# Performance work log

Measured on AMD Instinct MI355X. Metric: run time of the kernel, lower is better.

The kernel has to match this reference:

```python
import jax, jax.numpy as jnp
import numpy as np

N_NODES = 50000
N_EDGES = 800000
IN_DIM, HID_DIM, OUT_DIM, N_CLASSES = 128, 256, 64, 40


def _xavier(key, shape):
    fan_in, fan_out = shape[0], shape[1]
    std = float(np.sqrt(2.0 / (fan_in + fan_out)))
    return jax.random.normal(key, shape, dtype=jnp.float32) * std


def gcn_conv(x, W, b, src, dst, n_nodes):
    """PyG GCNConv: add self-loops, symmetric D^-1/2 (A+I) D^-1/2 X W + b."""
    h = x @ W  # [N, out]
    loop = jnp.arange(n_nodes, dtype=src.dtype)
    s = jnp.concatenate([src, loop])  # sources (messages flow src -> dst)
    d = jnp.concatenate([dst, loop])
    ones = jnp.ones(s.shape[0], dtype=h.dtype)
    deg = jax.ops.segment_sum(ones, d, num_segments=n_nodes)  # in-degree incl. self-loop
    dinv = jnp.where(deg > 0, jax.lax.rsqrt(deg), 0.0)
    norm = dinv[s] * dinv[d]  # [E+N]
    msg = h[s] * norm[:, None]
    out = jax.ops.segment_sum(msg, d, num_segments=n_nodes)
    return out + b


def setup_inputs() -> dict:
    key = jax.random.key(0)
    ks = jax.random.split(key, 9)
    x = jax.random.normal(ks[0], (N_NODES, IN_DIM), dtype=jnp.float32)
    edge_index = jax.random.randint(ks[1], (2, N_EDGES), 0, N_NODES, dtype=jnp.int64)
    return {
        "x": x,
        "edge_index": edge_index,
        "W1": _xavier(ks[2], (IN_DIM, HID_DIM)),
        "b1": jnp.zeros((HID_DIM,), jnp.float32),
        "W2": _xavier(ks[3], (HID_DIM, OUT_DIM)),
        "b2": jnp.zeros((OUT_DIM,), jnp.float32),
        "Wp1": _xavier(ks[4], (2 * OUT_DIM, 4 * OUT_DIM)),
        "bp1": jnp.zeros((4 * OUT_DIM,), jnp.float32),
        "Wp2": _xavier(ks[5], (4 * OUT_DIM, OUT_DIM)),
        "bp2": jnp.zeros((OUT_DIM,), jnp.float32),
        "Wc": _xavier(ks[6], (OUT_DIM, N_CLASSES)),
        "bc": jnp.zeros((N_CLASSES,), jnp.float32),
    }


def reference(x, edge_index, W1, b1, W2, b2, Wp1, bp1, Wp2, bp2, Wc, bc):
    src, dst = edge_index[0], edge_index[1]
    n = x.shape[0]
    h = jax.nn.relu(gcn_conv(x, W1, b1, src, dst, n))  # [N, HID]
    f = gcn_conv(h, W2, b2, src, dst, n)  # [N, OUT]
    # edge MLP on gathered endpoint features
    ef = jnp.concatenate([f[src], f[dst]], axis=-1)  # [E, 2*OUT]
    ef = jax.nn.relu(ef @ Wp1 + bp1)  # [E, 4*OUT]
    edge_feats = ef @ Wp2 + bp2  # [E, OUT]
    logits = f @ Wc + bc  # [N, C]
    return f, edge_feats, logits, edge_index
```

## Files before the change

kernel.cpp:

```cpp
#include <hip/hip_runtime.h>

#define N_NODES   50000
#define N_EDGES   800000
#define IN_DIM    128
#define HID_DIM   256
#define OUT_DIM   64
#define N_CLASSES 40

typedef __attribute__((ext_vector_type(8))) short short8;
typedef __attribute__((ext_vector_type(8))) unsigned short ushort8;
typedef __attribute__((ext_vector_type(4))) float f32x4;

__device__ inline short f2bf(float x) {
    unsigned u = __builtin_bit_cast(unsigned, x);
    unsigned r = (u + 0x7FFFu + ((u >> 16) & 1u)) >> 16;
    return (short)r;
}
__device__ inline float bf2f(unsigned short u) {
    unsigned v = ((unsigned)u) << 16;
    return __builtin_bit_cast(float, v);
}
__device__ inline unsigned cvtpk(float lo, float hi) {
    unsigned r;
    asm("v_cvt_pk_bf16_f32 %0, %1, %2" : "=v"(r) : "v"(lo), "v"(hi));
    return r;
}
__device__ __host__ inline int swap23(int p) {
    return (p & 0xC3) | ((p >> 2) & 0x0C) | ((p << 2) & 0x30);
}


__global__ void k_prep(const float* __restrict__ x, const int* __restrict__ ei,
                       const float* __restrict__ W1, const float* __restrict__ W2,
                       const float* __restrict__ Wp1, const float* __restrict__ Wp2,
                       unsigned short* __restrict__ xb,
                       short* __restrict__ W1t, short* __restrict__ W2t,
                       short* __restrict__ Wp1t, short* __restrict__ Wp2t,
                       int* __restrict__ degi, int* __restrict__ cursor,
                       float* __restrict__ ei_out) {
    int i = blockIdx.x * 256 + threadIdx.x;
    if (i < N_NODES) { degi[i] = 0; cursor[i] = 0; }
    if (i < 128 * 256) {
        int k = i >> 8, n = i & 255;
        W1t[n * 128 + k]  = f2bf(W1[i]);
        Wp1t[n * 128 + k] = f2bf(Wp1[i]);
    }
    if (i < 256 * 64) {
        int p = i >> 6, o = i & 63;
        int h = swap23(p);
        W2t[o * 256 + p]  = f2bf(W2[h * 64 + o]);
        Wp2t[o * 256 + p] = f2bf(Wp2[h * 64 + o]);
    }
    if (i < N_NODES * IN_DIM / 4) {
        float4 v = ((const float4*)x)[i];
        uint2 u;
        u.x = cvtpk(v.x, v.y);
        u.y = cvtpk(v.z, v.w);
        *(uint2*)((unsigned short*)xb + (size_t)i * 4) = u;
    }
    if (i < (2 * N_EDGES) / 4) {
        int4 v = ((const int4*)ei)[i];
        float4 o = {(float)v.x, (float)v.y, (float)v.z, (float)v.w};
        ((float4*)ei_out)[i] = o;
    }
}


__global__ void k_deg_count(const int* __restrict__ dst, int* __restrict__ degi) {
    int e = blockIdx.x * 256 + threadIdx.x;
    if (e < N_EDGES) atomicAdd(&degi[dst[e]], 1);
}

__global__ void k_scan_bsum(const int* __restrict__ vals, int n, int* __restrict__ bsum,
                            float* __restrict__ dinv) {
    __shared__ int sm[256];
    int t = threadIdx.x, i = blockIdx.x * 256 + t;
    int d = (i < n) ? vals[i] : 0;
    if (i < n) dinv[i] = rsqrtf((float)(d + 1));
    sm[t] = d;
    __syncthreads();
    for (int s = 128; s > 0; s >>= 1) {
        if (t < s) sm[t] += sm[t + s];
        __syncthreads();
    }
    if (t == 0) bsum[blockIdx.x] = sm[0];
}

__global__ void k_scan_bscan(int* __restrict__ bsum, int nb) {
    __shared__ int sm[256];
    int t = threadIdx.x;
    int orig = (t < nb) ? bsum[t] : 0;
    sm[t] = orig;
    __syncthreads();
    for (int off = 1; off < 256; off <<= 1) {
        int v = (t >= off) ? sm[t - off] : 0;
        __syncthreads();
        sm[t] += v;
        __syncthreads();
    }
    if (t < nb) bsum[t] = sm[t] - orig;
}

__global__ void k_scan_final(const int* __restrict__ vals, int n,
                             const int* __restrict__ bscan, int* __restrict__ out) {
    __shared__ int sm[256];
    int t = threadIdx.x, i = blockIdx.x * 256 + t;
    int orig = (i < n) ? vals[i] : 0;
    sm[t] = orig;
    __syncthreads();
    for (int off = 1; off < 256; off <<= 1) {
        int v = (t >= off) ? sm[t - off] : 0;
        __syncthreads();
        sm[t] += v;
        __syncthreads();
    }
    int excl = sm[t] - orig + bscan[blockIdx.x];
    if (i < n) out[i] = excl;
    if (i == n - 1) out[n] = excl + orig;
}

__global__ void k_csr_fill(const int* __restrict__ src, const int* __restrict__ dst,
                           const int* __restrict__ csr_off, int* __restrict__ cursor,
                           int* __restrict__ csr_src) {
    int e = blockIdx.x * 256 + threadIdx.x;
    if (e < N_EDGES) {
        int d = dst[e];
        int pos = csr_off[d] + atomicAdd(&cursor[d], 1);
        csr_src[pos] = src[e];
    }
}


__global__ __launch_bounds__(256) void k_agg0(const unsigned short* __restrict__ xb,
                                              const float* __restrict__ dinv,
                                              const int* __restrict__ csr_off,
                                              const int* __restrict__ csr_src,
                                              unsigned short* __restrict__ xa) {
    const int v = blockIdx.x * 4 + (threadIdx.x >> 6);
    const int lane = threadIdx.x & 63;
    float dv = dinv[v];
    unsigned c = *(const unsigned*)(xb + (size_t)v * 128 + lane * 2);
    float a0 = bf2f((unsigned short)(c & 0xFFFF)) * dv;
    float a1 = bf2f((unsigned short)(c >> 16)) * dv;
    int beg = csr_off[v], end = csr_off[v + 1];
    for (int base = beg; base < end; base += 64) {
        int idx = base + lane;
        int sj = (idx < end) ? csr_src[idx] : 0;
        float dj = (idx < end) ? dinv[sj] : 0.f;
        int m = min(64, end - base);
        int j = 0;
        for (; j + 4 <= m; j += 4) {
            int s0 = __shfl(sj, j), s1 = __shfl(sj, j + 1);
            int s2 = __shfl(sj, j + 2), s3 = __shfl(sj, j + 3);
            float d0 = __shfl(dj, j), d1 = __shfl(dj, j + 1);
            float d2 = __shfl(dj, j + 2), d3 = __shfl(dj, j + 3);
            unsigned h0 = *(const unsigned*)(xb + (size_t)s0 * 128 + lane * 2);
            unsigned h1 = *(const unsigned*)(xb + (size_t)s1 * 128 + lane * 2);
            unsigned h2 = *(const unsigned*)(xb + (size_t)s2 * 128 + lane * 2);
            unsigned h3 = *(const unsigned*)(xb + (size_t)s3 * 128 + lane * 2);
            a0 += bf2f((unsigned short)(h0 & 0xFFFF)) * d0 + bf2f((unsigned short)(h1 & 0xFFFF)) * d1
                + bf2f((unsigned short)(h2 & 0xFFFF)) * d2 + bf2f((unsigned short)(h3 & 0xFFFF)) * d3;
            a1 += bf2f((unsigned short)(h0 >> 16)) * d0 + bf2f((unsigned short)(h1 >> 16)) * d1
                + bf2f((unsigned short)(h2 >> 16)) * d2 + bf2f((unsigned short)(h3 >> 16)) * d3;
        }
        for (; j < m; j++) {
            int s = __shfl(sj, j);
            float ds = __shfl(dj, j);
            unsigned hv = *(const unsigned*)(xb + (size_t)s * 128 + lane * 2);
            a0 += bf2f((unsigned short)(hv & 0xFFFF)) * ds;
            a1 += bf2f((unsigned short)(hv >> 16)) * ds;
        }
    }
    *(unsigned*)(xa + (size_t)v * 128 + lane * 2) = cvtpk(a0 * dv, a1 * dv);
}


__global__ __launch_bounds__(256) void k_agg2(const unsigned short* __restrict__ h2b,
                                              const float* __restrict__ dinv,
                                              const int* __restrict__ csr_off,
                                              const int* __restrict__ csr_src,
                                              const float* __restrict__ b2,
                                              const float* __restrict__ Wc,
                                              const float* __restrict__ bc,
                                              float* __restrict__ f_out,
                                              unsigned short* __restrict__ fb,
                                              float* __restrict__ lg_out) {
    const int v = blockIdx.x * 4 + (threadIdx.x >> 6);
    const int lane = threadIdx.x & 63;
    float dv = dinv[v];
    float acc = bf2f(h2b[(size_t)v * 64 + lane]) * dv;
    int beg = csr_off[v], end = csr_off[v + 1];
    for (int base = beg; base < end; base += 64) {
        int idx = base + lane;
        int sj = (idx < end) ? csr_src[idx] : 0;
        float dj = (idx < end) ? dinv[sj] : 0.f;
        int m = min(64, end - base);
        int j = 0;
        for (; j + 4 <= m; j += 4) {
            int s0 = __shfl(sj, j), s1 = __shfl(sj, j + 1);
            int s2 = __shfl(sj, j + 2), s3 = __shfl(sj, j + 3);
            float d0 = __shfl(dj, j), d1 = __shfl(dj, j + 1);
            float d2 = __shfl(dj, j + 2), d3 = __shfl(dj, j + 3);
            float h0 = bf2f(h2b[(size_t)s0 * 64 + lane]);
            float h1 = bf2f(h2b[(size_t)s1 * 64 + lane]);
            float h2 = bf2f(h2b[(size_t)s2 * 64 + lane]);
            float h3 = bf2f(h2b[(size_t)s3 * 64 + lane]);
            acc += h0 * d0 + h1 * d1 + h2 * d2 + h3 * d3;
        }
        for (; j < m; j++) {
            int s = __shfl(sj, j);
            float ds = __shfl(dj, j);
            acc += bf2f(h2b[(size_t)s * 64 + lane]) * ds;
        }
    }
    float r = acc * dv + b2[lane];
    f_out[(size_t)v * 64 + lane] = r;
    fb[(size_t)v * 64 + lane] = (unsigned short)f2bf(r);
    bool act = lane < N_CLASSES;
    float lacc = act ? bc[lane] : 0.f;
    #pragma unroll
    for (int i2 = 0; i2 < 64; i2++) {
        float fi = __shfl(r, i2);
        if (act) lacc += fi * Wc[i2 * N_CLASSES + lane];
    }
    if (act) lg_out[(size_t)v * N_CLASSES + lane] = lacc;
}


__global__ __launch_bounds__(256) void k_gemm12(const unsigned short* __restrict__ xa,
                                                const short* __restrict__ W1t,
                                                const float* __restrict__ b1,
                                                const short* __restrict__ W2t,
                                                unsigned short* __restrict__ h2b) {
    __shared__ unsigned short xs[64 * 128];
    __shared__ unsigned short hs[64 * 256];
    const int t = threadIdx.x;
    const int lane = t & 63, wv = t >> 6, lr = lane & 15, lg = lane >> 4;
    const int nb = blockIdx.x * 64;

    #pragma unroll
    for (int i = 0; i < 4; i++) {
        int q = t + i * 256, row = q >> 4, seg = q & 15;
        int node = nb + row;
        ushort8 v = {0, 0, 0, 0, 0, 0, 0, 0};
        if (node < N_NODES) v = *(const ushort8*)(xa + (size_t)node * 128 + seg * 8);
        *(ushort8*)((char*)xs + ((row * 256 + seg * 16) ^ ((row & 7) << 4))) = v;
    }

    short8 A1[4][4];
    #pragma unroll
    for (int mi = 0; mi < 4; mi++)
        #pragma unroll
        for (int kt = 0; kt < 4; kt++)
            A1[mi][kt] = *(const short8*)(W1t + (size_t)(wv * 64 + mi * 16 + lr) * 128 + kt * 32 + lg * 8);
    float4 bb1[4];
    #pragma unroll
    for (int mi = 0; mi < 4; mi++)
        bb1[mi] = *(const float4*)(b1 + wv * 64 + mi * 16 + lg * 4);
    __syncthreads();

    #pragma unroll
    for (int nj = 0; nj < 4; nj++) {
        short8 Bf[4];
        int nr = nj * 16 + lr;
        #pragma unroll
        for (int kt = 0; kt < 4; kt++)
            Bf[kt] = *(const short8*)((const char*)xs + ((nr * 256 + kt * 64 + lg * 16) ^ ((nr & 7) << 4)));
        #pragma unroll
        for (int mh = 0; mh < 2; mh++) {
            f32x4 a0 = {0.f, 0.f, 0.f, 0.f}, a1 = {0.f, 0.f, 0.f, 0.f};
            #pragma unroll
            for (int kt = 0; kt < 4; kt++) {
                a0 = __builtin_amdgcn_mfma_f32_16x16x32_bf16(A1[mh * 2 + 0][kt], Bf[kt], a0, 0, 0, 0);
                a1 = __builtin_amdgcn_mfma_f32_16x16x32_bf16(A1[mh * 2 + 1][kt], Bf[kt], a1, 0, 0, 0);
            }
            float4 b0 = bb1[mh * 2 + 0], b1v = bb1[mh * 2 + 1];
            uint4 pkv;
            pkv.x = cvtpk(fmaxf(a0[0] + b0.x, 0.f),  fmaxf(a0[1] + b0.y, 0.f));
            pkv.y = cvtpk(fmaxf(a0[2] + b0.z, 0.f),  fmaxf(a0[3] + b0.w, 0.f));
            pkv.z = cvtpk(fmaxf(a1[0] + b1v.x, 0.f), fmaxf(a1[1] + b1v.y, 0.f));
            pkv.w = cvtpk(fmaxf(a1[2] + b1v.z, 0.f), fmaxf(a1[3] + b1v.w, 0.f));
            *(uint4*)((char*)hs + ((nr * 512 + wv * 128 + lg * 32 + mh * 16) ^ ((nr & 7) << 4))) = pkv;
        }
    }

    short8 A2[8];
    #pragma unroll
    for (int kt = 0; kt < 8; kt++)
        A2[kt] = *(const short8*)(W2t + (size_t)(wv * 16 + lr) * 256 + kt * 32 + lg * 8);
    asm volatile("s_waitcnt lgkmcnt(0)" ::: "memory");
    __builtin_amdgcn_s_barrier();

    #pragma unroll
    for (int nj = 0; nj < 4; nj++) {
        short8 Bh[8];
        int nr = nj * 16 + lr;
        #pragma unroll
        for (int kt = 0; kt < 8; kt++)
            Bh[kt] = *(const short8*)((const char*)hs + ((nr * 512 + kt * 64 + lg * 16) ^ ((nr & 7) << 4)));
        int node = nb + nr;
        f32x4 acc = {0.f, 0.f, 0.f, 0.f};
        #pragma unroll
        for (int kt = 0; kt < 8; kt++)
            acc = __builtin_amdgcn_mfma_f32_16x16x32_bf16(A2[kt], Bh[kt], acc, 0, 0, 0);
        if (node < N_NODES) {
            uint2 u;
            u.x = cvtpk(acc[0], acc[1]);
            u.y = cvtpk(acc[2], acc[3]);
            *(uint2*)(h2b + (size_t)node * 64 + wv * 16 + lg * 4) = u;
        }
    }
}


__global__ __launch_bounds__(256) void k_edge_mlpC(
        const unsigned short* __restrict__ fb,
        const int* __restrict__ src, const int* __restrict__ dst,
        const short* __restrict__ Wp1t, const float* __restrict__ bp1,
        const short* __restrict__ Wp2t, const float* __restrict__ bp2,
        float* __restrict__ out, int n_tiles) {
    __shared__ unsigned short hid_s[2][32 * 256];

    const int t = threadIdx.x;
    const int lane = t & 63, wv = t >> 6, lr = lane & 15, lg = lane >> 4;

    short8 A1[4][4];
    #pragma unroll
    for (int mi = 0; mi < 4; mi++)
        #pragma unroll
        for (int kt = 0; kt < 4; kt++)
            A1[mi][kt] = *(const short8*)(Wp1t + (size_t)(wv * 64 + mi * 16 + lr) * 128 + kt * 32 + lg * 8);
    short8 A2[8];
    #pragma unroll
    for (int kt = 0; kt < 8; kt++)
        A2[kt] = *(const short8*)(Wp2t + (size_t)(wv * 16 + lr) * 256 + kt * 32 + lg * 8);
    float4 bb1[4];
    #pragma unroll
    for (int mi = 0; mi < 4; mi++)
        bb1[mi] = *(const float4*)(bp1 + wv * 64 + mi * 16 + lg * 4);
    const float4 bv2 = *(const float4*)(bp2 + wv * 16 + lg * 4);

    int tile = blockIdx.x;
    if (tile >= n_tiles) return;
    const int g = gridDim.x;

    short8 Bf[2][4];
    {
        int sC[2], dC[2];
        #pragma unroll
        for (int nj = 0; nj < 2; nj++) {
            int e = tile * 32 + nj * 16 + lr;
            sC[nj] = src[e];
            dC[nj] = dst[e];
        }
        #pragma unroll
        for (int nj = 0; nj < 2; nj++) {
            const unsigned short* srow = fb + (size_t)sC[nj] * 64;
            const unsigned short* drow = fb + (size_t)dC[nj] * 64;
            Bf[nj][0] = *(const short8*)(srow + lg * 8);
            Bf[nj][1] = *(const short8*)(srow + 32 + lg * 8);
            Bf[nj][2] = *(const short8*)(drow + lg * 8);
            Bf[nj][3] = *(const short8*)(drow + 32 + lg * 8);
        }
    }
    int sA[2], dA[2];
    {
        int tn = tile + g;
        if (tn < n_tiles) {
            #pragma unroll
            for (int nj = 0; nj < 2; nj++) {
                int e = tn * 32 + nj * 16 + lr;
                sA[nj] = src[e];
                dA[nj] = dst[e];
            }
        }
    }

    int cur = 0;
    for (; tile < n_tiles; tile += g) {
        #pragma unroll
        for (int nj = 0; nj < 2; nj++) {
            int er = nj * 16 + lr;
            #pragma unroll
            for (int mh = 0; mh < 2; mh++) {
                f32x4 a0 = {0.f, 0.f, 0.f, 0.f}, a1 = {0.f, 0.f, 0.f, 0.f};
                #pragma unroll
                for (int kt = 0; kt < 4; kt++) {
                    a0 = __builtin_amdgcn_mfma_f32_16x16x32_bf16(A1[mh * 2 + 0][kt], Bf[nj][kt], a0, 0, 0, 0);
                    a1 = __builtin_amdgcn_mfma_f32_16x16x32_bf16(A1[mh * 2 + 1][kt], Bf[nj][kt], a1, 0, 0, 0);
                }
                float4 b0 = bb1[mh * 2 + 0], b1v = bb1[mh * 2 + 1];
                uint4 pkv;
                pkv.x = cvtpk(fmaxf(a0[0] + b0.x, 0.f),  fmaxf(a0[1] + b0.y, 0.f));
                pkv.y = cvtpk(fmaxf(a0[2] + b0.z, 0.f),  fmaxf(a0[3] + b0.w, 0.f));
                pkv.z = cvtpk(fmaxf(a1[0] + b1v.x, 0.f), fmaxf(a1[1] + b1v.y, 0.f));
                pkv.w = cvtpk(fmaxf(a1[2] + b1v.z, 0.f), fmaxf(a1[3] + b1v.w, 0.f));
                *(uint4*)((char*)hid_s[cur] +
                    ((er * 512 + wv * 128 + lg * 32 + mh * 16) ^ ((er & 7) << 4))) = pkv;
            }
        }

        int tn = tile + g;
        if (tn < n_tiles) {
            #pragma unroll
            for (int nj = 0; nj < 2; nj++) {
                const unsigned short* srow = fb + (size_t)sA[nj] * 64;
                const unsigned short* drow = fb + (size_t)dA[nj] * 64;
                Bf[nj][0] = *(const short8*)(srow + lg * 8);
                Bf[nj][1] = *(const short8*)(srow + 32 + lg * 8);
                Bf[nj][2] = *(const short8*)(drow + lg * 8);
                Bf[nj][3] = *(const short8*)(drow + 32 + lg * 8);
            }
        }
        int tnn = tile + 2 * g;
        if (tnn < n_tiles) {
            #pragma unroll
            for (int nj = 0; nj < 2; nj++) {
                int e = tnn * 32 + nj * 16 + lr;
                sA[nj] = src[e];
                dA[nj] = dst[e];
            }
        }

        asm volatile("s_waitcnt lgkmcnt(0)" ::: "memory");
        __builtin_amdgcn_s_barrier();

        #pragma unroll
        for (int nj = 0; nj < 2; nj++) {
            short8 Bh[8];
            int er = nj * 16 + lr;
            #pragma unroll
            for (int kt = 0; kt < 8; kt++)
                Bh[kt] = *(const short8*)((const char*)hid_s[cur] +
                             ((er * 512 + kt * 64 + lg * 16) ^ ((er & 7) << 4)));
            f32x4 acc = {0.f, 0.f, 0.f, 0.f};
            #pragma unroll
            for (int kt = 0; kt < 8; kt++)
                acc = __builtin_amdgcn_mfma_f32_16x16x32_bf16(A2[kt], Bh[kt], acc, 0, 0, 0);
            float4 o = {acc[0] + bv2.x, acc[1] + bv2.y, acc[2] + bv2.z, acc[3] + bv2.w};
            *(float4*)(out + (size_t)(tile * 32 + er) * 64 + wv * 16 + lg * 4) = o;
        }
        cur ^= 1;
    }
}


extern "C" void kernel_launch(void* const* d_in, const int* in_sizes, int n_in,
                              void* d_out, int out_size, void* d_ws, size_t ws_size,
                              hipStream_t stream) {
    const float* x   = (const float*)d_in[0];
    const int*   ei  = (const int*)d_in[1];
    const float* W1  = (const float*)d_in[2];
    const float* b1  = (const float*)d_in[3];
    const float* W2  = (const float*)d_in[4];
    const float* b2  = (const float*)d_in[5];
    const float* Wp1 = (const float*)d_in[6];
    const float* bp1 = (const float*)d_in[7];
    const float* Wp2 = (const float*)d_in[8];
    const float* bp2 = (const float*)d_in[9];
    const float* Wc  = (const float*)d_in[10];
    const float* bc  = (const float*)d_in[11];

    const int* src = ei;
    const int* dst = ei + N_EDGES;

    float* out    = (float*)d_out;
    float* f_out  = out;
    float* ef_out = out + (size_t)N_NODES * OUT_DIM;
    float* lg_out = ef_out + (size_t)N_EDGES * OUT_DIM;
    float* ei_out = lg_out + (size_t)N_NODES * N_CLASSES;

    char* p = (char*)d_ws;
    auto alloc = [&](size_t bytes) -> char* {
        char* r = p;
        p += (bytes + 255) / 256 * 256;
        return r;
    };
    unsigned short* xb   = (unsigned short*)alloc((size_t)N_NODES * IN_DIM * 2);
    unsigned short* xa   = (unsigned short*)alloc((size_t)N_NODES * IN_DIM * 2);
    unsigned short* h2b  = (unsigned short*)alloc((size_t)N_NODES * OUT_DIM * 2);
    unsigned short* fb   = (unsigned short*)alloc((size_t)N_NODES * OUT_DIM * 2);
    int*   degi    = (int*)alloc((size_t)N_NODES * 4);
    float* dinv    = (float*)alloc((size_t)N_NODES * 4);
    int*   csr_off = (int*)alloc((size_t)(N_NODES + 1) * 4);
    int*   cursor  = (int*)alloc((size_t)N_NODES * 4);
    int*   csr_src = (int*)alloc((size_t)N_EDGES * 4);
    int*   bsum    = (int*)alloc(256 * 4);
    short* W1t     = (short*)alloc((size_t)256 * 128 * 2);
    short* W2t     = (short*)alloc((size_t)64 * 256 * 2);
    short* Wp1t    = (short*)alloc((size_t)256 * 128 * 2);
    short* Wp2t    = (short*)alloc((size_t)64 * 256 * 2);

    const int nbScan = (N_NODES + 255) / 256;

    k_prep<<<(N_NODES * IN_DIM / 4 + 255) / 256, 256, 0, stream>>>(
        x, ei, W1, W2, Wp1, Wp2, xb, W1t, W2t, Wp1t, Wp2t, degi, cursor, ei_out);
    k_deg_count<<<(N_EDGES + 255) / 256, 256, 0, stream>>>(dst, degi);
    k_scan_bsum<<<nbScan, 256, 0, stream>>>(degi, N_NODES, bsum, dinv);
    k_scan_bscan<<<1, 256, 0, stream>>>(bsum, nbScan);
    k_scan_final<<<nbScan, 256, 0, stream>>>(degi, N_NODES, bsum, csr_off);
    k_csr_fill<<<(N_EDGES + 255) / 256, 256, 0, stream>>>(src, dst, csr_off, cursor, csr_src);

    const int nbG = (N_NODES + 63) / 64;
    k_agg0<<<N_NODES / 4, 256, 0, stream>>>(xb, dinv, csr_off, csr_src, xa);
    k_gemm12<<<nbG, 256, 0, stream>>>(xa, W1t, b1, W2t, h2b);
    k_agg2<<<N_NODES / 4, 256, 0, stream>>>(h2b, dinv, csr_off, csr_src, b2, Wc, bc,
                                            f_out, fb, lg_out);

    k_edge_mlpC<<<1280, 256, 0, stream>>>(fb, src, dst, Wp1t, bp1, Wp2t, bp2,
                                          ef_out, N_EDGES / 32);
}
```

Before: 372.9 us.

## Deepen edge MLP gather prefetch to two tiles with double register buffers

Restructures the edge-MLP loop to process two tiles per iteration with separate register buffers, so endpoint feature rows are gathered two tiles ahead instead of one. The grid shrinks from 1280 to 768 blocks, giving each block more tiles to amortise its weight loads. This aims to hide the latency of the random row gathers. The extra register buffers raise VGPR pressure and may lower occupancy.

Result: slower. 390.3 us (+4.6%).

```diff
diff --git a/kernel.cpp b/kernel.cpp
--- a/kernel.cpp
+++ b/kernel.cpp
@@ -313,7 +313,7 @@
 }
 
 
-__global__ __launch_bounds__(256) void k_edge_mlpC(
+__global__ __launch_bounds__(256) void k_edge_mlpD(
         const unsigned short* __restrict__ fb,
         const int* __restrict__ src, const int* __restrict__ dst,
         const short* __restrict__ Wp1t, const float* __restrict__ bp1,
@@ -340,44 +340,33 @@
         bb1[mi] = *(const float4*)(bp1 + wv * 64 + mi * 16 + lg * 4);
     const float4 bv2 = *(const float4*)(bp2 + wv * 16 + lg * 4);
 
-    int tile = blockIdx.x;
-    if (tile >= n_tiles) return;
     const int g = gridDim.x;
-
-    short8 Bf[2][4];
-    {
-        int sC[2], dC[2];
+    const int t0 = blockIdx.x;
+    if (t0 >= n_tiles) return;
+
+    short8 BfA[2][4], BfB[2][4];
+    int sA[2], dA[2];
+
+    auto loadIdx = [&](int tl, int* s, int* d) {
         #pragma unroll
         for (int nj = 0; nj < 2; nj++) {
-            int e = tile * 32 + nj * 16 + lr;
-            sC[nj] = src[e];
-            dC[nj] = dst[e];
-        }
+            int e = tl * 32 + nj * 16 + lr;
+            s[nj] = src[e];
+            d[nj] = dst[e];
+        }
+    };
+    auto loadRows = [&](const int* s, const int* d, short8 Bf[2][4]) {
         #pragma unroll
         for (int nj = 0; nj < 2; nj++) {
-            const unsigned short* srow = fb + (size_t)sC[nj] * 64;
-            const unsigned short* drow = fb + (size_t)dC[nj] * 64;
+            const unsigned short* srow = fb + (size_t)s[nj] * 64;
+            const unsigned short* drow = fb + (size_t)d[nj] * 64;
             Bf[nj][0] = *(const short8*)(srow + lg * 8);
             Bf[nj][1] = *(const short8*)(srow + 32 + lg * 8);
             Bf[nj][2] = *(const short8*)(drow + lg * 8);
             Bf[nj][3] = *(const short8*)(drow + 32 + lg * 8);
         }
-    }
-    int sA[2], dA[2];
-    {
-        int tn = tile + g;
-        if (tn < n_tiles) {
-            #pragma unroll
-            for (int nj = 0; nj < 2; nj++) {
-                int e = tn * 32 + nj * 16 + lr;
-                sA[nj] = src[e];
-                dA[nj] = dst[e];
-            }
-        }
-    }
-
-    int cur = 0;
-    for (; tile < n_tiles; tile += g) {
+    };
+    auto phaseL1 = [&](short8 Bf[2][4], unsigned short* hid) {
         #pragma unroll
         for (int nj = 0; nj < 2; nj++) {
             int er = nj * 16 + lr;
@@ -395,43 +384,18 @@
                 pkv.y = cvtpk(fmaxf(a0[2] + b0.z, 0.f),  fmaxf(a0[3] + b0.w, 0.f));
                 pkv.z = cvtpk(fmaxf(a1[0] + b1v.x, 0.f), fmaxf(a1[1] + b1v.y, 0.f));
                 pkv.w = cvtpk(fmaxf(a1[2] + b1v.z, 0.f), fmaxf(a1[3] + b1v.w, 0.f));
-                *(uint4*)((char*)hid_s[cur] +
-                    ((er * 512 + wv * 128 + lg * 32 + mh * 16) ^ ((er & 7) << 4))) = pkv;
+                *(uint4*)((char*)hid + ((er * 512 + wv * 128 + lg * 32 + mh * 16) ^ ((er & 7) << 4))) = pkv;
             }
         }
-
-        int tn = tile + g;
-        if (tn < n_tiles) {
-            #pragma unroll
-            for (int nj = 0; nj < 2; nj++) {
-                const unsigned short* srow = fb + (size_t)sA[nj] * 64;
-                const unsigned short* drow = fb + (size_t)dA[nj] * 64;
-                Bf[nj][0] = *(const short8*)(srow + lg * 8);
-                Bf[nj][1] = *(const short8*)(srow + 32 + lg * 8);
-                Bf[nj][2] = *(const short8*)(drow + lg * 8);
-                Bf[nj][3] = *(const short8*)(drow + 32 + lg * 8);
-            }
-        }
-        int tnn = tile + 2 * g;
-        if (tnn < n_tiles) {
-            #pragma unroll
-            for (int nj = 0; nj < 2; nj++) {
-                int e = tnn * 32 + nj * 16 + lr;
-                sA[nj] = src[e];
-                dA[nj] = dst[e];
-            }
-        }
-
-        asm volatile("s_waitcnt lgkmcnt(0)" ::: "memory");
-        __builtin_amdgcn_s_barrier();
-
+    };
+    auto phaseL2 = [&](const unsigned short* hid, int tile) {
         #pragma unroll
         for (int nj = 0; nj < 2; nj++) {
             short8 Bh[8];
             int er = nj * 16 + lr;
             #pragma unroll
             for (int kt = 0; kt < 8; kt++)
-                Bh[kt] = *(const short8*)((const char*)hid_s[cur] +
+                Bh[kt] = *(const short8*)((const char*)hid +
                              ((er * 512 + kt * 64 + lg * 16) ^ ((er & 7) << 4)));
             f32x4 acc = {0.f, 0.f, 0.f, 0.f};
             #pragma unroll
@@ -440,7 +404,36 @@
             float4 o = {acc[0] + bv2.x, acc[1] + bv2.y, acc[2] + bv2.z, acc[3] + bv2.w};
             *(float4*)(out + (size_t)(tile * 32 + er) * 64 + wv * 16 + lg * 4) = o;
         }
-        cur ^= 1;
+    };
+
+    {
+        int si[2], di[2];
+        loadIdx(t0, si, di);
+        loadRows(si, di, BfA);
+        if (t0 + g < n_tiles) {
+            loadIdx(t0 + g, si, di);
+            loadRows(si, di, BfB);
+        }
+        if (t0 + 2 * g < n_tiles) loadIdx(t0 + 2 * g, sA, dA);
+    }
+
+    for (int tile = t0; tile < n_tiles; tile += 2 * g) {
+        phaseL1(BfA, hid_s[0]);
+        if (tile + 2 * g < n_tiles) loadRows(sA, dA, BfA);
+        if (tile + 3 * g < n_tiles) loadIdx(tile + 3 * g, sA, dA);
+        asm volatile("s_waitcnt lgkmcnt(0)" ::: "memory");
+        __builtin_amdgcn_s_barrier();
+        phaseL2(hid_s[0], tile);
+
+        int tb = tile + g;
+        if (tb < n_tiles) {
+            phaseL1(BfB, hid_s[1]);
+            if (tb + 2 * g < n_tiles) loadRows(sA, dA, BfB);
+            if (tb + 3 * g < n_tiles) loadIdx(tb + 3 * g, sA, dA);
+            asm volatile("s_waitcnt lgkmcnt(0)" ::: "memory");
+            __builtin_amdgcn_s_barrier();
+            phaseL2(hid_s[1], tb);
+        }
     }
 }
 
@@ -507,6 +500,6 @@
     k_agg2<<<N_NODES / 4, 256, 0, stream>>>(h2b, dinv, csr_off, csr_src, b2, Wc, bc,
                                             f_out, fb, lg_out);
 
-    k_edge_mlpC<<<1280, 256, 0, stream>>>(fb, src, dst, Wp1t, bp1, Wp2t, bp2,
-                                          ef_out, N_EDGES / 32);
-}
+    k_edge_mlpD<<<768, 256, 0, stream>>>(fb, src, dst, Wp1t, bp1, Wp2t, bp2,
+                                         ef_out, N_EDGES / 32);
+}
```
